# Kernel optimization log

Hardware: AMD Instinct MI355X
Metric: run time of the kernel (lower is better)

The kernel has to match this reference:

```python
import jax, jax.numpy as jnp
import numpy as np
import math

B, S, D, H = 8, 1024, 768, 12
DEPTH = D // H
MAX_LEN = 1024


def setup_inputs() -> dict:
    key = jax.random.key(0)
    ks = jax.random.split(key, 16)
    inp = {
        "Q": jax.random.normal(ks[0], (B, S, D), dtype=jnp.float32),
        "K": jax.random.normal(ks[1], (B, S, D), dtype=jnp.float32),
        "V": jax.random.normal(ks[2], (B, S, D), dtype=jnp.float32),
        # additive mask: 1 where attention is disallowed (causal upper triangle)
        "mask": jnp.triu(jnp.ones((S, S), dtype=jnp.float32), k=1)[None, None],
        "Wq": jax.random.normal(ks[3], (D, D), dtype=jnp.float32) / math.sqrt(D),
        "bq": jnp.zeros((D,), dtype=jnp.float32),
        "Wk": jax.random.normal(ks[4], (D, D), dtype=jnp.float32) / math.sqrt(D),
        "bk": jnp.zeros((D,), dtype=jnp.float32),
        "Wv": jax.random.normal(ks[5], (D, D), dtype=jnp.float32) / math.sqrt(D),
        "bv": jnp.zeros((D,), dtype=jnp.float32),
        "Wo": jax.random.normal(ks[6], (D, D), dtype=jnp.float32) / math.sqrt(D),
        "bo": jnp.zeros((D,), dtype=jnp.float32),
        "Er": jax.random.normal(ks[7], (MAX_LEN, DEPTH), dtype=jnp.float32),
    }
    return inp


def _skew(QEr):
    # QEr: [B,H,S,S] -> pad one zero col on the left, reshape, drop first row
    b, h, s, _ = QEr.shape
    padded = jnp.pad(QEr, ((0, 0), (0, 0), (0, 0), (1, 0)))  # [B,H,S,S+1]
    reshaped = padded.reshape(b, h, s + 1, s)
    return reshaped[:, :, 1:, :]  # [B,H,S,S]


def reference(Q, K, V, mask, Wq, bq, Wk, bk, Wv, bv, Wo, bo, Er):
    batch, seq, d_model = Q.shape
    q = (Q @ Wq.T + bq).reshape(batch, seq, H, DEPTH).transpose(0, 2, 1, 3)
    k = (K @ Wk.T + bk).reshape(batch, seq, H, DEPTH).transpose(0, 2, 1, 3)
    v = (V @ Wv.T + bv).reshape(batch, seq, H, DEPTH).transpose(0, 2, 1, 3)

    # relative position bias via skew trick
    QEr = jnp.einsum('bhsd,td->bhst', q, Er[:seq])
    Srel = _skew(QEr)

    logits = (jnp.einsum('bhsd,bhtd->bhst', q, k) + Srel) / math.sqrt(DEPTH)
    logits = logits + mask * (-1e9)
    attn = jax.nn.softmax(logits, axis=-1)  # [B,H,S,S]
    out = jnp.einsum('bhst,bhtd->bhsd', attn, v)
    out = out.transpose(0, 2, 1, 3).reshape(batch, seq, d_model)
    out = out @ Wo.T + bo
    return out
```

## Files before the change

### kernel.cpp

```cpp
#include <hip/hip_runtime.h>

typedef __bf16 bf16_t;
typedef __bf16 bf16x8 __attribute__((ext_vector_type(8)));
typedef float  f32x4  __attribute__((ext_vector_type(4)));

#define MFMA16(a, b, c) __builtin_amdgcn_mfma_f32_16x16x32_bf16((a), (b), (c), 0, 0, 0)
#define LOG2E 1.44269504f

#define DPP_ROR(x, N) __int_as_float(__builtin_amdgcn_update_dpp( \
    0, __float_as_int(x), 0x120 + (N), 0xF, 0xF, true))

__device__ inline bf16x8 load8(const bf16_t* p) { return *(const bf16x8*)p; }
__device__ inline bf16x8 load8(const float* p) {
    f32x4 a = *(const f32x4*)p;
    f32x4 b = *(const f32x4*)(p + 4);
    bf16x8 r;
    r[0] = (bf16_t)a[0]; r[1] = (bf16_t)a[1]; r[2] = (bf16_t)a[2]; r[3] = (bf16_t)a[3];
    r[4] = (bf16_t)b[0]; r[5] = (bf16_t)b[1]; r[6] = (bf16_t)b[2]; r[7] = (bf16_t)b[3];
    return r;
}

__global__ void cvt_er(const float* __restrict__ Er, bf16_t* __restrict__ Erb)
{
    const int idx = blockIdx.x * 256 + threadIdx.x;
    Erb[idx] = (idx < 65536) ? (bf16_t)Er[idx] : (bf16_t)0.0f;
}

template <typename XT, typename WT, typename OT>
__device__ __forceinline__ void
gemm128(const XT* __restrict__ X, const WT* __restrict__ W,
        const float* __restrict__ bias, OT* __restrict__ Out, int mode,
        int m0, int n0, bf16_t (*Al)[72], bf16_t (*Bl)[72])
{
    const int tid  = threadIdx.x;
    const int w    = tid >> 6;
    const int lane = tid & 63;
    const int quad = lane >> 4;
    const int l16  = lane & 15;
    const int wr   = (w >> 1) * 64;
    const int wc   = (w & 1) * 64;

    f32x4 acc[4][4];
#pragma unroll
    for (int mi = 0; mi < 4; ++mi)
#pragma unroll
        for (int ni = 0; ni < 4; ++ni)
#pragma unroll
            for (int r = 0; r < 4; ++r) acc[mi][ni][r] = 0.0f;

    const int srow = tid >> 3;
    const int scol = (tid & 7) * 8;

    for (int kc = 0; kc < 12; ++kc) {
        const int k0 = kc * 64;
        __syncthreads();
#pragma unroll
        for (int p = 0; p < 4; ++p) {
            const int row = p * 32 + srow;
            *(bf16x8*)&Al[row][scol] = load8(X + (size_t)(m0 + row) * 768 + k0 + scol);
            *(bf16x8*)&Bl[row][scol] = load8(W + (size_t)(n0 + row) * 768 + k0 + scol);
        }
        __syncthreads();
#pragma unroll
        for (int kk = 0; kk < 2; ++kk) {
            bf16x8 a[4], b[4];
#pragma unroll
            for (int mi = 0; mi < 4; ++mi)
                a[mi] = *(const bf16x8*)&Al[wr + mi * 16 + l16][kk * 32 + quad * 8];
#pragma unroll
            for (int ni = 0; ni < 4; ++ni)
                b[ni] = *(const bf16x8*)&Bl[wc + ni * 16 + l16][kk * 32 + quad * 8];
#pragma unroll
            for (int mi = 0; mi < 4; ++mi)
#pragma unroll
                for (int ni = 0; ni < 4; ++ni)
                    acc[mi][ni] = MFMA16(a[mi], b[ni], acc[mi][ni]);
        }
    }

#pragma unroll
    for (int ni = 0; ni < 4; ++ni) {
        const int n  = n0 + wc + ni * 16 + l16;
        const float bn = bias[n];
#pragma unroll
        for (int mi = 0; mi < 4; ++mi) {
#pragma unroll
            for (int r = 0; r < 4; ++r) {
                const int m = m0 + wr + mi * 16 + quad * 4 + r;
                const float v = acc[mi][ni][r] + bn;
                if (mode == 0) {
                    const int bb = m >> 10, ss = m & 1023, hh = n >> 6, dd = n & 63;
                    Out[(((size_t)(bb * 12 + hh)) * 1024 + ss) * 64 + dd] = (OT)v;
                } else if (mode == 2) {
                    const int bb = m >> 10, ss = m & 1023, hh = n >> 6, dd = n & 63;
                    Out[(((size_t)(bb * 12 + hh)) * 64 + dd) * 1024 + ss] = (OT)v;
                } else {
                    Out[(size_t)m * 768 + n] = (OT)v;
                }
            }
        }
    }
}

__global__ void __launch_bounds__(256)
qkv_proj(const float* __restrict__ Q, const float* __restrict__ K,
         const float* __restrict__ V,
         const float* __restrict__ Wq, const float* __restrict__ Wk,
         const float* __restrict__ Wv,
         const float* __restrict__ bq, const float* __restrict__ bk,
         const float* __restrict__ bv,
         bf16_t* __restrict__ qo, bf16_t* __restrict__ ko, bf16_t* __restrict__ vo)
{
    __shared__ bf16_t Al[128][72];
    __shared__ bf16_t Bl[128][72];
    const int z = blockIdx.z;
    const float* X  = (z == 0) ? Q  : (z == 1) ? K  : V;
    const float* W  = (z == 0) ? Wq : (z == 1) ? Wk : Wv;
    const float* bs = (z == 0) ? bq : (z == 1) ? bk : bv;
    bf16_t* Out     = (z == 0) ? qo : (z == 1) ? ko : vo;
    gemm128<float, float, bf16_t>(X, W, bs, Out, (z == 2) ? 2 : 0,
                                  blockIdx.x * 128, blockIdx.y * 128, Al, Bl);
}

__global__ void __launch_bounds__(256)
out_proj(const bf16_t* __restrict__ X, const float* __restrict__ W,
         const float* __restrict__ bias, float* __restrict__ Out)
{
    __shared__ bf16_t Al[128][72];
    __shared__ bf16_t Bl[128][72];
    gemm128<bf16_t, float, float>(X, W, bias, Out, 1,
                                  blockIdx.x * 128, blockIdx.y * 128, Al, Bl);
}

__global__ void __launch_bounds__(256)
attn_kernel(const bf16_t* __restrict__ qb, const bf16_t* __restrict__ kb,
            const bf16_t* __restrict__ vt, const bf16_t* __restrict__ Erb,
            bf16_t* __restrict__ att)
{
    __shared__ bf16_t Kl[64][72];
    __shared__ bf16_t Vtl[64][72];
    __shared__ bf16_t Erl[128][72];
    __shared__ bf16_t Pl[4][16][72];

    const int tid  = threadIdx.x;
    const int bid  = blockIdx.x;
    const int bh   = bid >> 3;
    const int pr   = bid & 7;
    const int b    = bh / 12;
    const int h    = bh % 12;
    const int w    = tid >> 6;
    const int lane = tid & 63;
    const int quad = lane >> 4;
    const int l16  = lane & 15;
    const int u0   = 48 - 16 * w;
    const int srow = tid >> 3;
    const int scol = (tid & 7) * 8;

    const bf16_t* qp = qb + (size_t)bh * 65536;
    const bf16_t* kp = kb + (size_t)bh * 65536;
    const bf16_t* vp = vt + (size_t)bh * 65536;

#pragma unroll 1
    for (int phase = 0; phase < 2; ++phase) {
        const int qt  = phase ? (15 - pr) : pr;
        const int s0  = qt * 64;
        const int s0w = s0 + 16 * w;
        const int E00 = 960 - s0;

        bf16x8 aq[2];
#pragma unroll
        for (int kk = 0; kk < 2; ++kk)
            aq[kk] = load8(qp + (size_t)(s0w + l16) * 64 + kk * 32 + quad * 8);

        __syncthreads();

#pragma unroll
        for (int p = 0; p < 2; ++p) {
            *(bf16x8*)&Kl[p * 32 + srow][scol]  = load8(kp + (size_t)(p * 32 + srow) * 64 + scol);
            *(bf16x8*)&Vtl[p * 32 + srow][scol] = load8(vp + (size_t)(p * 32 + srow) * 1024 + scol);
        }
#pragma unroll
        for (int p = 0; p < 4; ++p) {
            const int e = E00 + p * 32 + srow;
            *(bf16x8*)&Erl[e & 127][scol] = load8(Erb + (size_t)e * 64 + scol);
        }
        __syncthreads();

        float mrow[4], lrow[4];
        f32x4 o[4];
#pragma unroll
        for (int r = 0; r < 4; ++r) { mrow[r] = -1e30f; lrow[r] = 0.0f; }
#pragma unroll
        for (int nt = 0; nt < 4; ++nt)
#pragma unroll
            for (int r = 0; r < 4; ++r) o[nt][r] = 0.0f;

        const int nT = qt + 1;
        for (int tt = 0; tt < nT; ++tt) {
            const int t0 = tt * 64;
            const int E0 = E00 + t0;
            const bool more = (tt + 1 < nT);

            bf16x8 kpre[2], vpre[2], epre[2];
            if (more) {
                const int t0n = t0 + 64;
#pragma unroll
                for (int p = 0; p < 2; ++p) {
                    kpre[p] = load8(kp + (size_t)(t0n + p * 32 + srow) * 64 + scol);
                    vpre[p] = load8(vp + (size_t)(p * 32 + srow) * 1024 + t0n + scol);
                    const int e = E0 + 128 + p * 32 + srow;
                    epre[p] = load8(Erb + (size_t)e * 64 + scol);
                }
            }

            f32x4 sacc[4], gacc[5];
#pragma unroll
            for (int nt = 0; nt < 4; ++nt)
#pragma unroll
                for (int r = 0; r < 4; ++r) sacc[nt][r] = 0.0f;
#pragma unroll
            for (int gt = 0; gt < 5; ++gt)
#pragma unroll
                for (int r = 0; r < 4; ++r) gacc[gt][r] = 0.0f;

            __builtin_amdgcn_s_setprio(1);
#pragma unroll
            for (int kk = 0; kk < 2; ++kk) {
#pragma unroll
                for (int nt = 0; nt < 4; ++nt) {
                    if (t0 + nt * 16 <= s0w + 15) {
                        bf16x8 bk_ = *(const bf16x8*)&Kl[nt * 16 + l16][kk * 32 + quad * 8];
                        sacc[nt] = MFMA16(aq[kk], bk_, sacc[nt]);
                    }
                }
#pragma unroll
                for (int gt = 0; gt < 5; ++gt) {
                    const int er = (E0 + u0 + gt * 16 + l16) & 127;
                    bf16x8 be = *(const bf16x8*)&Erl[er][kk * 32 + quad * 8];
                    gacc[gt] = MFMA16(aq[kk], be, gacc[gt]);
                }
            }
            __builtin_amdgcn_s_setprio(0);

#pragma unroll
            for (int r = 0; r < 4; ++r) {
                const int i   = quad * 4 + r;
                const int cc  = 15 - i + l16;
                const int src = (lane & 48) | (cc & 15);
                const bool lo = (cc < 16);
                float rot[5];
#pragma unroll
                for (int gt = 0; gt < 5; ++gt) rot[gt] = __shfl(gacc[gt][r], src);
#pragma unroll
                for (int nt = 0; nt < 4; ++nt) {
                    const float g = lo ? rot[nt] : rot[nt + 1];
                    float sv = (sacc[nt][r] + g) * 0.125f;
                    if (t0 + nt * 16 + l16 > s0w + i) sv = -1e9f;
                    sacc[nt][r] = sv;
                }
            }

#pragma unroll
            for (int r = 0; r < 4; ++r) {
                float vm = fmaxf(fmaxf(sacc[0][r], sacc[1][r]), fmaxf(sacc[2][r], sacc[3][r]));
                vm = fmaxf(vm, DPP_ROR(vm, 8));
                vm = fmaxf(vm, DPP_ROR(vm, 4));
                vm = fmaxf(vm, DPP_ROR(vm, 2));
                vm = fmaxf(vm, DPP_ROR(vm, 1));
                const float mnew  = fmaxf(mrow[r], vm);
                const float alpha = __builtin_exp2f((mrow[r] - mnew) * LOG2E);
                mrow[r] = mnew;
                float rs = 0.0f;
#pragma unroll
                for (int nt = 0; nt < 4; ++nt) {
                    const float p_ = __builtin_exp2f((sacc[nt][r] - mnew) * LOG2E);
                    sacc[nt][r] = p_;
                    rs += p_;
                }
                rs += DPP_ROR(rs, 8);
                rs += DPP_ROR(rs, 4);
                rs += DPP_ROR(rs, 2);
                rs += DPP_ROR(rs, 1);
                lrow[r] = lrow[r] * alpha + rs;
                o[0][r] *= alpha; o[1][r] *= alpha;
                o[2][r] *= alpha; o[3][r] *= alpha;
            }

#pragma unroll
            for (int nt = 0; nt < 4; ++nt)
#pragma unroll
                for (int r = 0; r < 4; ++r)
                    Pl[w][quad * 4 + r][nt * 16 + l16] = (bf16_t)sacc[nt][r];

            __builtin_amdgcn_s_setprio(1);
#pragma unroll
            for (int kk = 0; kk < 2; ++kk) {
                bf16x8 ap = *(const bf16x8*)&Pl[w][l16][kk * 32 + quad * 8];
#pragma unroll
                for (int nt = 0; nt < 4; ++nt) {
                    bf16x8 bv_ = *(const bf16x8*)&Vtl[nt * 16 + l16][kk * 32 + quad * 8];
                    o[nt] = MFMA16(ap, bv_, o[nt]);
                }
            }
            __builtin_amdgcn_s_setprio(0);

            if (more) {
                __syncthreads();
#pragma unroll
                for (int p = 0; p < 2; ++p) {
                    *(bf16x8*)&Kl[p * 32 + srow][scol]  = kpre[p];
                    *(bf16x8*)&Vtl[p * 32 + srow][scol] = vpre[p];
                    const int e = E0 + p * 32 + srow;
                    *(bf16x8*)&Erl[e & 127][scol] = epre[p];
                }
                __syncthreads();
            }
        }

#pragma unroll
        for (int nt = 0; nt < 4; ++nt) {
#pragma unroll
            for (int r = 0; r < 4; ++r) {
                const int s_idx = s0w + quad * 4 + r;
                const int d     = nt * 16 + l16;
                att[((size_t)b * 1024 + s_idx) * 768 + h * 64 + d] = (bf16_t)(o[nt][r] / lrow[r]);
            }
        }
    }
}

extern "C" void kernel_launch(void* const* d_in, const int* in_sizes, int n_in,
                              void* d_out, int out_size, void* d_ws, size_t ws_size,
                              hipStream_t stream)
{
    const float* Q  = (const float*)d_in[0];
    const float* K  = (const float*)d_in[1];
    const float* V  = (const float*)d_in[2];
    const float* Wq = (const float*)d_in[4];
    const float* bq = (const float*)d_in[5];
    const float* Wk = (const float*)d_in[6];
    const float* bk = (const float*)d_in[7];
    const float* Wv = (const float*)d_in[8];
    const float* bv = (const float*)d_in[9];
    const float* Wo = (const float*)d_in[10];
    const float* bo = (const float*)d_in[11];
    const float* Er = (const float*)d_in[12];
    float* out      = (float*)d_out;

    const size_t per = (size_t)8 * 12 * 1024 * 64;
    bf16_t* qbuf  = (bf16_t*)d_out;
    bf16_t* Erb   = qbuf + per;
    bf16_t* kbuf  = (bf16_t*)d_ws;
    bf16_t* vtbuf = kbuf + per;
    bf16_t* abuf  = vtbuf + per;

    cvt_er<<<dim3(288), dim3(256), 0, stream>>>(Er, Erb);
    qkv_proj<<<dim3(64, 6, 3), dim3(256), 0, stream>>>(Q, K, V, Wq, Wk, Wv,
                                                       bq, bk, bv, qbuf, kbuf, vtbuf);
    attn_kernel<<<dim3(768), dim3(256), 0, stream>>>(qbuf, kbuf, vtbuf, Erb, abuf);
    out_proj<<<dim3(64, 6), dim3(256), 0, stream>>>(abuf, Wo, bo, out);
}
```

Before: 348.0 us.

## Pre-convert inputs and weights to bf16 and stage GEMM tiles via global_load_lds

Adds a single conversion kernel that turns Q, K, V, all four weight matrices and Er into bf16 buffers up front. The projection GEMMs then read bf16 and stage tiles into LDS with direct global-to-LDS loads, using a per-8-row padded layout. This removes in-loop fp32 loads and conversions and cuts VGPR staging traffic. In exchange it adds an extra pass over the inputs, writing and re-reading about 19 MB of bf16, plus more workspace reuse (abuf aliases kxb).

```diff
diff --git a/kernel.cpp b/kernel.cpp
--- a/kernel.cpp
+++ b/kernel.cpp
@@ -20,17 +20,41 @@
     return r;
 }
 
-__global__ void cvt_er(const float* __restrict__ Er, bf16_t* __restrict__ Erb)
+__global__ void __launch_bounds__(256)
+cvt_all(const float* __restrict__ Q, const float* __restrict__ K,
+        const float* __restrict__ V, const float* __restrict__ Wq,
+        const float* __restrict__ Wk, const float* __restrict__ Wv,
+        const float* __restrict__ Wo, const float* __restrict__ Er,
+        bf16_t* __restrict__ qxb, bf16_t* __restrict__ kxb,
+        bf16_t* __restrict__ vxb, bf16_t* __restrict__ wqb,
+        bf16_t* __restrict__ wkb, bf16_t* __restrict__ wvb,
+        bf16_t* __restrict__ wob, bf16_t* __restrict__ Erb)
 {
     const int idx = blockIdx.x * 256 + threadIdx.x;
-    Erb[idx] = (idx < 65536) ? (bf16_t)Er[idx] : (bf16_t)0.0f;
-}
-
-template <typename XT, typename WT, typename OT>
+    const float* src;  bf16_t* dst;  int off;
+    if      (idx <  786432) { src = Q;  dst = qxb; off = idx; }
+    else if (idx < 1572864) { src = K;  dst = kxb; off = idx -  786432; }
+    else if (idx < 2359296) { src = V;  dst = vxb; off = idx - 1572864; }
+    else if (idx < 2433024) { src = Wq; dst = wqb; off = idx - 2359296; }
+    else if (idx < 2506752) { src = Wk; dst = wkb; off = idx - 2433024; }
+    else if (idx < 2580480) { src = Wv; dst = wvb; off = idx - 2506752; }
+    else if (idx < 2654208) { src = Wo; dst = wob; off = idx - 2580480; }
+    else {
+        off = idx - 2654208;
+        bf16x8 r;
+        if (off < 8192) r = load8(Er + (size_t)off * 8);
+        else { for (int j = 0; j < 8; ++j) r[j] = (bf16_t)0.0f; }
+        *(bf16x8*)(Erb + (size_t)off * 8) = r;
+        return;
+    }
+    *(bf16x8*)(dst + (size_t)off * 8) = load8(src + (size_t)off * 8);
+}
+
+template <typename OT>
 __device__ __forceinline__ void
-gemm128(const XT* __restrict__ X, const WT* __restrict__ W,
+gemm_bt(const bf16_t* __restrict__ X, const bf16_t* __restrict__ W,
         const float* __restrict__ bias, OT* __restrict__ Out, int mode,
-        int m0, int n0, bf16_t (*Al)[72], bf16_t (*Bl)[72])
+        int m0, int n0, bf16_t* Al, bf16_t* Bl)
 {
     const int tid  = threadIdx.x;
     const int w    = tid >> 6;
@@ -39,6 +63,8 @@
     const int l16  = lane & 15;
     const int wr   = (w >> 1) * 64;
     const int wc   = (w & 1) * 64;
+    const int l8r  = lane >> 3;
+    const int l8c  = lane & 7;
 
     f32x4 acc[4][4];
 #pragma unroll
@@ -48,28 +74,35 @@
 #pragma unroll
             for (int r = 0; r < 4; ++r) acc[mi][ni][r] = 0.0f;
 
-    const int srow = tid >> 3;
-    const int scol = (tid & 7) * 8;
+    const bf16_t* gA = X + (size_t)(m0 + w * 32 + l8r) * 768 + l8c * 8;
+    const bf16_t* gB = W + (size_t)(n0 + w * 32 + l8r) * 768 + l8c * 8;
 
     for (int kc = 0; kc < 12; ++kc) {
         const int k0 = kc * 64;
         __syncthreads();
 #pragma unroll
         for (int p = 0; p < 4; ++p) {
-            const int row = p * 32 + srow;
-            *(bf16x8*)&Al[row][scol] = load8(X + (size_t)(m0 + row) * 768 + k0 + scol);
-            *(bf16x8*)&Bl[row][scol] = load8(W + (size_t)(n0 + row) * 768 + k0 + scol);
+            __builtin_amdgcn_global_load_lds(
+                (__attribute__((address_space(1))) const void*)(gA + (size_t)p * 8 * 768 + k0),
+                (__attribute__((address_space(3))) void*)(Al + (w * 4 + p) * 528), 16, 0, 0);
+            __builtin_amdgcn_global_load_lds(
+                (__attribute__((address_space(1))) const void*)(gB + (size_t)p * 8 * 768 + k0),
+                (__attribute__((address_space(3))) void*)(Bl + (w * 4 + p) * 528), 16, 0, 0);
         }
         __syncthreads();
 #pragma unroll
         for (int kk = 0; kk < 2; ++kk) {
             bf16x8 a[4], b[4];
 #pragma unroll
-            for (int mi = 0; mi < 4; ++mi)
-                a[mi] = *(const bf16x8*)&Al[wr + mi * 16 + l16][kk * 32 + quad * 8];
-#pragma unroll
-            for (int ni = 0; ni < 4; ++ni)
-                b[ni] = *(const bf16x8*)&Bl[wc + ni * 16 + l16][kk * 32 + quad * 8];
+            for (int mi = 0; mi < 4; ++mi) {
+                const int row = wr + mi * 16 + l16;
+                a[mi] = *(const bf16x8*)&Al[(row >> 3) * 528 + (row & 7) * 64 + kk * 32 + quad * 8];
+            }
+#pragma unroll
+            for (int ni = 0; ni < 4; ++ni) {
+                const int row = wc + ni * 16 + l16;
+                b[ni] = *(const bf16x8*)&Bl[(row >> 3) * 528 + (row & 7) * 64 + kk * 32 + quad * 8];
+            }
 #pragma unroll
             for (int mi = 0; mi < 4; ++mi)
 #pragma unroll
@@ -103,33 +136,32 @@
 }
 
 __global__ void __launch_bounds__(256)
-qkv_proj(const float* __restrict__ Q, const float* __restrict__ K,
-         const float* __restrict__ V,
-         const float* __restrict__ Wq, const float* __restrict__ Wk,
-         const float* __restrict__ Wv,
+qkv_proj(const bf16_t* __restrict__ Qx, const bf16_t* __restrict__ Kx,
+         const bf16_t* __restrict__ Vx,
+         const bf16_t* __restrict__ Wq, const bf16_t* __restrict__ Wk,
+         const bf16_t* __restrict__ Wv,
          const float* __restrict__ bq, const float* __restrict__ bk,
          const float* __restrict__ bv,
          bf16_t* __restrict__ qo, bf16_t* __restrict__ ko, bf16_t* __restrict__ vo)
 {
-    __shared__ bf16_t Al[128][72];
-    __shared__ bf16_t Bl[128][72];
+    __shared__ bf16_t Al[16 * 528];
+    __shared__ bf16_t Bl[16 * 528];
     const int z = blockIdx.z;
-    const float* X  = (z == 0) ? Q  : (z == 1) ? K  : V;
-    const float* W  = (z == 0) ? Wq : (z == 1) ? Wk : Wv;
-    const float* bs = (z == 0) ? bq : (z == 1) ? bk : bv;
-    bf16_t* Out     = (z == 0) ? qo : (z == 1) ? ko : vo;
-    gemm128<float, float, bf16_t>(X, W, bs, Out, (z == 2) ? 2 : 0,
-                                  blockIdx.x * 128, blockIdx.y * 128, Al, Bl);
+    const bf16_t* X  = (z == 0) ? Qx : (z == 1) ? Kx : Vx;
+    const bf16_t* W  = (z == 0) ? Wq : (z == 1) ? Wk : Wv;
+    const float* bs  = (z == 0) ? bq : (z == 1) ? bk : bv;
+    bf16_t* Out      = (z == 0) ? qo : (z == 1) ? ko : vo;
+    gemm_bt<bf16_t>(X, W, bs, Out, (z == 2) ? 2 : 0,
+                    blockIdx.x * 128, blockIdx.y * 128, Al, Bl);
 }
 
 __global__ void __launch_bounds__(256)
-out_proj(const bf16_t* __restrict__ X, const float* __restrict__ W,
+out_proj(const bf16_t* __restrict__ X, const bf16_t* __restrict__ W,
          const float* __restrict__ bias, float* __restrict__ Out)
 {
-    __shared__ bf16_t Al[128][72];
-    __shared__ bf16_t Bl[128][72];
-    gemm128<bf16_t, float, float>(X, W, bias, Out, 1,
-                                  blockIdx.x * 128, blockIdx.y * 128, Al, Bl);
+    __shared__ bf16_t Al[16 * 528];
+    __shared__ bf16_t Bl[16 * 528];
+    gemm_bt<float>(X, W, bias, Out, 1, blockIdx.x * 128, blockIdx.y * 128, Al, Bl);
 }
 
 __global__ void __launch_bounds__(256)
@@ -348,15 +380,27 @@
     float* out      = (float*)d_out;
 
     const size_t per = (size_t)8 * 12 * 1024 * 64;
-    bf16_t* qbuf  = (bf16_t*)d_out;
-    bf16_t* Erb   = qbuf + per;
+    const size_t wsz = (size_t)768 * 768;
+
+    bf16_t* qxb   = (bf16_t*)d_out;
+    bf16_t* qbuf  = qxb + per;
+
     bf16_t* kbuf  = (bf16_t*)d_ws;
     bf16_t* vtbuf = kbuf + per;
-    bf16_t* abuf  = vtbuf + per;
-
-    cvt_er<<<dim3(288), dim3(256), 0, stream>>>(Er, Erb);
-    qkv_proj<<<dim3(64, 6, 3), dim3(256), 0, stream>>>(Q, K, V, Wq, Wk, Wv,
+    bf16_t* kxb   = vtbuf + per;
+    bf16_t* vxb   = kxb + per;
+    bf16_t* wqb   = vxb + per;
+    bf16_t* wkb   = wqb + wsz;
+    bf16_t* wvb   = wkb + wsz;
+    bf16_t* wob   = wvb + wsz;
+    bf16_t* Erb   = wob + wsz;
+    bf16_t* abuf  = kxb;
+
+    cvt_all<<<dim3(10404), dim3(256), 0, stream>>>(Q, K, V, Wq, Wk, Wv, Wo, Er,
+                                                   qxb, kxb, vxb, wqb, wkb, wvb,
+                                                   wob, Erb);
+    qkv_proj<<<dim3(64, 6, 3), dim3(256), 0, stream>>>(qxb, kxb, vxb, wqb, wkb, wvb,
                                                        bq, bk, bv, qbuf, kbuf, vtbuf);
     attn_kernel<<<dim3(768), dim3(256), 0, stream>>>(qbuf, kbuf, vtbuf, Erb, abuf);
-    out_proj<<<dim3(64, 6), dim3(256), 0, stream>>>(abuf, Wo, bo, out);
-}
+    out_proj<<<dim3(64, 6), dim3(256), 0, stream>>>(abuf, wob, bo, out);
+}
```

New measurement: 308.9 us. 1.13x faster.
